# Kernel optimization log

Hardware: AMD Instinct MI355X
Metric: run time of the kernel (lower is better)

The kernel has to match this reference:

```python
import jax, jax.numpy as jnp
import numpy as np

B, N, NPOINT, NSAMPLE = 8, 4096, 1024, 32
IN_CH = 29
MLP = [64, 64, 128]
D_IN = IN_CH + 3  # 32
D_OUT = 128
EPS = 1e-5


def setup_inputs() -> dict:
    key = jax.random.key(0)
    ks = jax.random.split(key, 32)
    inp = {}
    inp["xyz"] = jax.random.normal(ks[0], (B, 3, N), jnp.float32)
    inp["points"] = jax.random.normal(ks[1], (B, IN_CH, N), jnp.float32)
    last = IN_CH + 3
    for i, oc in enumerate(MLP):
        inp[f"mlp_w{i}"] = jax.random.normal(ks[2 + i], (oc, last), jnp.float32) * np.sqrt(2.0 / last).astype(np.float32)
        inp[f"mlp_b{i}"] = jnp.zeros((oc,), jnp.float32)
        inp[f"mlp_g{i}"] = jnp.ones((oc,), jnp.float32)
        inp[f"mlp_be{i}"] = jnp.zeros((oc,), jnp.float32)
        last = oc
    inp["conv1_w"] = jax.random.normal(ks[10], (D_OUT // 2, 4), jnp.float32) * np.float32(np.sqrt(2.0 / 4))
    inp["conv1_b"] = jnp.zeros((D_OUT // 2,), jnp.float32)
    inp["bn1_g"] = jnp.ones((D_OUT // 2,), jnp.float32)
    inp["bn1_be"] = jnp.zeros((D_OUT // 2,), jnp.float32)
    inp["conv2_w"] = jax.random.normal(ks[11], (D_OUT // 2, D_IN), jnp.float32) * np.float32(np.sqrt(2.0 / D_IN))
    inp["conv2_b"] = jnp.zeros((D_OUT // 2,), jnp.float32)
    inp["bn2_g"] = jnp.ones((D_OUT // 2,), jnp.float32)
    inp["bn2_be"] = jnp.zeros((D_OUT // 2,), jnp.float32)
    return inp


def _conv1x1(x, w, b):
    # x: [B,Cin,ns,S], w: [Cout,Cin] -> [B,Cout,ns,S]
    return jnp.einsum("bcns,oc->bons", x, w) + b[None, :, None, None]


def _bn_relu(x, g, be):
    # training-mode BatchNorm2d: batch stats over (B, ns, S), biased variance
    m = jnp.mean(x, axis=(0, 2, 3), keepdims=True)
    v = jnp.var(x, axis=(0, 2, 3), keepdims=True)
    y = g[None, :, None, None] * (x - m) * jax.lax.rsqrt(v + EPS) + be[None, :, None, None]
    return jax.nn.relu(y)


def _fps(xyz):
    # xyz: [B,N,3] -> centroid indices [B,NPOINT]; deterministic start at index 0
    Bn, Nn, _ = xyz.shape

    def step(carry, _):
        dist, far = carry
        cen = jnp.take_along_axis(xyz, far[:, None, None], axis=1)  # [B,1,3]
        d = jnp.sum((xyz - cen) ** 2, axis=-1)                      # [B,N]
        dist = jnp.minimum(dist, d)
        new_far = jnp.argmax(dist, axis=-1).astype(jnp.int32)
        return (dist, new_far), far

    init = (jnp.full((Bn, Nn), 1e10, xyz.dtype), jnp.zeros((Bn,), jnp.int32))
    _, cents = jax.lax.scan(step, init, None, length=NPOINT)
    return cents.T  # [B,NPOINT]


def _forward(xyz, points, mlp_params, conv1_w, conv1_b, bn1_g, bn1_be,
             conv2_w, conv2_b, bn2_g, bn2_be):
    xyz_t = xyz.transpose(0, 2, 1)      # [B,N,3]
    pts_t = points.transpose(0, 2, 1)   # [B,N,C]
    xyz_sg = jax.lax.stop_gradient(xyz_t)

    ct_idx = _fps(xyz_sg)                                   # [B,S]
    bidx = jnp.arange(B)[:, None]
    ct_xyz = xyz_t[bidx, ct_idx]                            # [B,S,3]

    # kNN via squared distances (indices only -> stop_gradient)
    ct_sg = jax.lax.stop_gradient(ct_xyz)
    d2 = (jnp.sum(ct_sg ** 2, -1)[:, :, None]
          + jnp.sum(xyz_sg ** 2, -1)[:, None, :]
          - 2.0 * jnp.einsum("bsc,bnc->bsn", ct_sg, xyz_sg))  # [B,S,N]
    _, gidx = jax.lax.top_k(-d2, NSAMPLE)                     # [B,S,ns]

    bidx3 = jnp.arange(B)[:, None, None]
    grouped_xyz = xyz_t[bidx3, gidx]                          # [B,S,ns,3]
    ft_xyz = grouped_xyz - ct_xyz[:, :, None, :]              # [B,S,ns,3]
    ft_points = jnp.concatenate([ft_xyz, pts_t[bidx3, gidx]], axis=-1)  # [B,S,ns,3+C]
    ft = ft_points.transpose(0, 3, 2, 1)                      # [B,3+C,ns,S]

    # shared MLP (conv-bn-relu stack), then max over neighbors
    x = ft
    for (w, b, g, be) in mlp_params:
        x = _bn_relu(_conv1x1(x, w, b), g, be)
    new_points1 = jnp.max(x, axis=2)                          # [B,mlp[-1],S]

    # relative positional encoding branch
    ct_p = ct_xyz.transpose(0, 2, 1)                          # [B,3,S]
    grouped_p = grouped_xyz.transpose(0, 3, 2, 1)             # [B,3,ns,S]
    rel = grouped_p - ct_p[:, :, None, :]                     # [B,3,ns,S]
    rd = jnp.sqrt(jnp.maximum(jnp.sum(rel ** 2, axis=1, keepdims=True), 1e-12))
    new_xyz = _bn_relu(_conv1x1(jnp.concatenate([rel, rd], axis=1), conv1_w, conv1_b), bn1_g, bn1_be)
    new_pts = _bn_relu(_conv1x1(ft, conv2_w, conv2_b), bn2_g, bn2_be)

    f_concat = jnp.concatenate([new_xyz, new_pts], axis=1)    # [B,d_out,ns,S]
    new_points2 = jnp.concatenate([jnp.mean(f_concat, axis=2), jnp.max(f_concat, axis=2)], axis=1)
    conv_points = jnp.concatenate([new_points1, new_points2], axis=1)  # [B,mlp[-1]+2*d_out,S]
    return ct_p, conv_points


def reference(xyz, points,
              mlp_w0, mlp_b0, mlp_g0, mlp_be0,
              mlp_w1, mlp_b1, mlp_g1, mlp_be1,
              mlp_w2, mlp_b2, mlp_g2, mlp_be2,
              conv1_w, conv1_b, bn1_g, bn1_be,
              conv2_w, conv2_b, bn2_g, bn2_be):
    mlp_params = [(mlp_w0, mlp_b0, mlp_g0, mlp_be0),
                  (mlp_w1, mlp_b1, mlp_g1, mlp_be1),
                  (mlp_w2, mlp_b2, mlp_g2, mlp_be2)]
    return _forward(xyz, points, mlp_params, conv1_w, conv1_b, bn1_g, bn1_be,
                    conv2_w, conv2_b, bn2_g, bn2_be)
```

## Files before the change

kernel.cpp:

```cpp
#include <hip/hip_runtime.h>
#include <cfloat>
#include <math.h>

constexpr int B_ = 8, N_ = 4096, S_ = 1024, NS_ = 32;
constexpr int R_ = B_ * S_ * NS_;
constexpr float EPS_ = 1e-5f;

__global__ __launch_bounds__(512) void fps_kernel(const float* __restrict__ xyz,
                                                  int* __restrict__ ct_idx) {
    int b = blockIdx.x;
    const float* xb = xyz + (size_t)b * 3 * N_;
    int t = threadIdx.x;
    __shared__ float sx[N_], sy[N_], sz[N_];
    __shared__ unsigned long long sb[2][8];
    for (int i = t; i < N_; i += 512) {
        sx[i] = xb[i];
        sy[i] = xb[N_ + i];
        sz[i] = xb[2 * N_ + i];
    }
    float px[8], py[8], pz[8], dist[8];
    unsigned inv_idx[8];
#pragma unroll
    for (int j = 0; j < 8; j++) {
        int n = j * 512 + t;
        px[j] = xb[n];
        py[j] = xb[N_ + n];
        pz[j] = xb[2 * N_ + n];
        dist[j] = 1e10f;
        inv_idx[j] = ~(unsigned)n;
    }
    __syncthreads();
    float cx = sx[0], cy = sy[0], cz = sz[0];
    int far = 0;
    for (int it = 0; it < S_; it++) {
        if (t == 0) ct_idx[b * S_ + it] = far;
        unsigned long long best = 0ull;
#pragma unroll
        for (int j = 0; j < 8; j++) {
            float dx = px[j] - cx, dy = py[j] - cy, dz = pz[j] - cz;
            float d = dx * dx + dy * dy + dz * dz;
            dist[j] = fminf(dist[j], d);
            unsigned long long pk =
                ((unsigned long long)__float_as_uint(dist[j]) << 32) | inv_idx[j];
            best = pk > best ? pk : best;
        }
#pragma unroll
        for (int m = 1; m < 64; m <<= 1) {
            unsigned long long o = __shfl_xor(best, m);
            best = o > best ? o : best;
        }
        int p = it & 1;
        if ((t & 63) == 0) sb[p][t >> 6] = best;
        __syncthreads();
#pragma unroll
        for (int w = 0; w < 8; w++) {
            unsigned long long o = sb[p][w];
            best = o > best ? o : best;
        }
        far = (int)(~(unsigned)(best & 0xffffffffu));
        cx = sx[far]; cy = sy[far]; cz = sz[far];
    }
}

__global__ __launch_bounds__(256) void knn_kernel(const float* __restrict__ xyz,
                                                  const int* __restrict__ ct_idx,
                                                  int* __restrict__ gidx) {
    int bs = blockIdx.x;
    int b = bs >> 10;
    const float* xb = xyz + (size_t)b * 3 * N_;
    int ci = ct_idx[bs];
    float cx = xb[ci], cy = xb[N_ + ci], cz = xb[2 * N_ + ci];
    float cs = cx * cx + cy * cy + cz * cz;
    int t = threadIdx.x;
    float val[16];
#pragma unroll
    for (int j = 0; j < 16; j++) {
        int n = j * 256 + t;
        float x = xb[n], y = xb[N_ + n], z = xb[2 * N_ + n];
        float xn = x * x + y * y + z * z;
        float dot = cx * x + cy * y + cz * z;
        val[j] = cs + xn - 2.f * dot;
    }
    __shared__ float sv[4];
    __shared__ int si[4];
    int out_base = bs * NS_;
    for (int iter = 0; iter < NS_; iter++) {
        float bv = FLT_MAX; int bi = 1 << 30;
#pragma unroll
        for (int j = 0; j < 16; j++) {
            if (val[j] < bv) { bv = val[j]; bi = j * 256 + t; }
        }
#pragma unroll
        for (int m = 1; m < 64; m <<= 1) {
            float ov = __shfl_xor(bv, m); int oi = __shfl_xor(bi, m);
            if (ov < bv || (ov == bv && oi < bi)) { bv = ov; bi = oi; }
        }
        if ((t & 63) == 0) { sv[t >> 6] = bv; si[t >> 6] = bi; }
        __syncthreads();
        bv = sv[0]; bi = si[0];
#pragma unroll
        for (int w = 1; w < 4; w++) {
            float ov = sv[w]; int oi = si[w];
            if (ov < bv || (ov == bv && oi < bi)) { bv = ov; bi = oi; }
        }
        if (t == 0) gidx[out_base + iter] = bi;
        if ((bi & 255) == t) val[bi >> 8] = FLT_MAX;
        __syncthreads();
    }
}

__global__ __launch_bounds__(256) void ctp_kernel(const float* __restrict__ xyz,
                                                  const int* __restrict__ ct_idx,
                                                  float* __restrict__ out) {
    int i = blockIdx.x * 256 + threadIdx.x;
    if (i >= B_ * 3 * S_) return;
    int b = i / (3 * S_);
    int rem = i - b * 3 * S_;
    int c = rem >> 10;
    int s = rem & (S_ - 1);
    int ci = ct_idx[b * S_ + s];
    out[i] = xyz[(size_t)b * 3 * N_ + (size_t)c * N_ + ci];
}

__global__ __launch_bounds__(256) void gather_kernel(const float* __restrict__ xyz,
                                                     const float* __restrict__ pts,
                                                     const int* __restrict__ ct_idx,
                                                     const int* __restrict__ gidx,
                                                     float* __restrict__ ft) {
    int r = blockIdx.x * 256 + threadIdx.x;
    int b = r >> 15;
    int s = (r >> 5) & (S_ - 1);
    int g = gidx[r];
    int ci = ct_idx[b * S_ + s];
    const float* xb = xyz + (size_t)b * 3 * N_;
    float rx = xb[g] - xb[ci];
    float ry = xb[N_ + g] - xb[N_ + ci];
    float rz = xb[2 * N_ + g] - xb[2 * N_ + ci];
    ft[r] = rx;
    ft[(size_t)R_ + r] = ry;
    ft[(size_t)2 * R_ + r] = rz;
    float rd = sqrtf(fmaxf(rx * rx + ry * ry + rz * rz, 1e-12f));
    ft[(size_t)32 * R_ + r] = rd;
    const float* pb = pts + (size_t)b * 29 * N_;
#pragma unroll
    for (int c = 0; c < 29; c++) ft[(size_t)(3 + c) * R_ + r] = pb[(size_t)c * N_ + g];
}

template <int CIN, bool AFF>
__global__ __launch_bounds__(256) void convk(const float* __restrict__ xin,
                                             const float* __restrict__ W,
                                             const float* __restrict__ bias,
                                             const float* __restrict__ ab,
                                             float* __restrict__ out0,
                                             float* __restrict__ out1) {
    __shared__ float Ws[CIN][64];
    __shared__ float bs[64];
    __shared__ float as_[CIN], bbs[CIN];
    int oc0 = blockIdx.y * 64;
    for (int i = threadIdx.x; i < CIN * 64; i += 256) {
        int o = i & 63, c = i >> 6;
        Ws[c][o] = W[(size_t)(oc0 + o) * CIN + c];
    }
    if (threadIdx.x < 64) bs[threadIdx.x] = bias[oc0 + threadIdx.x];
    if (AFF) {
        for (int i = threadIdx.x; i < CIN; i += 256) { as_[i] = ab[i]; bbs[i] = ab[CIN + i]; }
    }
    __syncthreads();
    size_t r0 = (size_t)blockIdx.x * 512 + threadIdx.x;
    float acc0[64], acc1[64];
#pragma unroll
    for (int o = 0; o < 64; o++) { acc0[o] = 0.f; acc1[o] = 0.f; }
    for (int c = 0; c < CIN; c++) {
        float x0 = xin[(size_t)c * R_ + r0];
        float x1 = xin[(size_t)c * R_ + r0 + 256];
        if (AFF) {
            float a = as_[c], bb = bbs[c];
            x0 = fmaxf(fmaf(a, x0, bb), 0.f);
            x1 = fmaxf(fmaf(a, x1, bb), 0.f);
        }
#pragma unroll
        for (int o = 0; o < 64; o++) {
            float w = Ws[c][o];
            acc0[o] = fmaf(x0, w, acc0[o]);
            acc1[o] = fmaf(x1, w, acc1[o]);
        }
    }
    float* outp = blockIdx.y ? out1 : out0;
#pragma unroll
    for (int o = 0; o < 64; o++) {
        float bv = bs[o];
        outp[(size_t)o * R_ + r0] = acc0[o] + bv;
        outp[(size_t)o * R_ + r0 + 256] = acc1[o] + bv;
    }
}

__global__ __launch_bounds__(256) void conv1_kernel(const float* __restrict__ ft,
                                                    const float* __restrict__ W,
                                                    const float* __restrict__ bias,
                                                    float* __restrict__ out) {
    __shared__ float Ws[4][64];
    __shared__ float bs[64];
    {
        int i = threadIdx.x;
        if (i < 256) { int o = i & 63, c = i >> 6; Ws[c][o] = W[o * 4 + c]; }
    }
    if (threadIdx.x < 64) bs[threadIdx.x] = bias[threadIdx.x];
    __syncthreads();
    size_t r0 = (size_t)blockIdx.x * 512 + threadIdx.x;
    float acc0[64], acc1[64];
#pragma unroll
    for (int o = 0; o < 64; o++) { acc0[o] = 0.f; acc1[o] = 0.f; }
    const int chs[4] = {0, 1, 2, 32};
#pragma unroll
    for (int c = 0; c < 4; c++) {
        int ch = chs[c];
        float x0 = ft[(size_t)ch * R_ + r0];
        float x1 = ft[(size_t)ch * R_ + r0 + 256];
#pragma unroll
        for (int o = 0; o < 64; o++) {
            float w = Ws[c][o];
            acc0[o] = fmaf(x0, w, acc0[o]);
            acc1[o] = fmaf(x1, w, acc1[o]);
        }
    }
#pragma unroll
    for (int o = 0; o < 64; o++) {
        float bv = bs[o];
        out[(size_t)o * R_ + r0] = acc0[o] + bv;
        out[(size_t)o * R_ + r0 + 256] = acc1[o] + bv;
    }
}

__global__ __launch_bounds__(256) void stats_partial(const float* __restrict__ y,
                                                     float* __restrict__ partial,
                                                     int cofs) {
    int c = blockIdx.x, p = blockIdx.y;
    const float* src = y + (size_t)c * R_ + (size_t)p * (R_ / 32);
    float s = 0.f, q = 0.f;
    for (int i = threadIdx.x; i < R_ / 32; i += 256) {
        float v = src[i];
        s += v;
        q = fmaf(v, v, q);
    }
#pragma unroll
    for (int m = 1; m < 64; m <<= 1) { s += __shfl_xor(s, m); q += __shfl_xor(q, m); }
    __shared__ float ls[4], lq[4];
    int w = threadIdx.x >> 6;
    if ((threadIdx.x & 63) == 0) { ls[w] = s; lq[w] = q; }
    __syncthreads();
    if (threadIdx.x == 0) {
        s = ls[0] + ls[1] + ls[2] + ls[3];
        q = lq[0] + lq[1] + lq[2] + lq[3];
        int idx = ((cofs + c) * 32 + p) * 2;
        partial[idx] = s;
        partial[idx + 1] = q;
    }
}

__global__ __launch_bounds__(64) void stats_final(const float* __restrict__ partial,
                                                  const float* __restrict__ g,
                                                  const float* __restrict__ be,
                                                  float* __restrict__ ab, int C) {
    int c = blockIdx.x, t = threadIdx.x;
    float s = 0.f, q = 0.f;
    if (t < 32) {
        int idx = (c * 32 + t) * 2;
        s = partial[idx];
        q = partial[idx + 1];
    }
#pragma unroll
    for (int m = 1; m < 32; m <<= 1) { s += __shfl_xor(s, m); q += __shfl_xor(q, m); }
    if (t == 0) {
        float inv = 1.0f / (float)R_;
        float mean = s * inv;
        float var = q * inv - mean * mean;
        float a = g[c] / sqrtf(var + EPS_);
        ab[c] = a;
        ab[C + c] = be[c] - mean * a;
    }
}

__global__ __launch_bounds__(128) void final_max(const float* __restrict__ yA,
                                                 const float* __restrict__ yC,
                                                 const float* __restrict__ ab,
                                                 float* __restrict__ out) {
    int bs = blockIdx.x;
    int c = threadIdx.x;
    const float* src = (c < 64 ? yA + (size_t)c * R_ : yC + (size_t)(c - 64) * R_) + (size_t)bs * NS_;
    float a = ab[c], bb = ab[128 + c];
    const float4* s4 = reinterpret_cast<const float4*>(src);
    float m = -FLT_MAX;
#pragma unroll
    for (int i = 0; i < 8; i++) {
        float4 v = s4[i];
        m = fmaxf(m, fmaxf(fmaf(a, v.x, bb), 0.f));
        m = fmaxf(m, fmaxf(fmaf(a, v.y, bb), 0.f));
        m = fmaxf(m, fmaxf(fmaf(a, v.z, bb), 0.f));
        m = fmaxf(m, fmaxf(fmaf(a, v.w, bb), 0.f));
    }
    int b = bs >> 10, s = bs & (S_ - 1);
    out[24576 + (size_t)b * 393216 + (size_t)c * 1024 + s] = m;
}

__global__ __launch_bounds__(128) void final_meanmax(const float* __restrict__ z1,
                                                     const float* __restrict__ z2,
                                                     const float* __restrict__ ab1,
                                                     const float* __restrict__ ab2,
                                                     float* __restrict__ out) {
    int bs = blockIdx.x;
    int c = threadIdx.x;
    const float* src;
    float a, bb;
    if (c < 64) { src = z1 + (size_t)c * R_; a = ab1[c]; bb = ab1[64 + c]; }
    else        { src = z2 + (size_t)(c - 64) * R_; a = ab2[c - 64]; bb = ab2[64 + (c - 64)]; }
    src += (size_t)bs * NS_;
    const float4* s4 = reinterpret_cast<const float4*>(src);
    float m = -FLT_MAX, sm = 0.f;
#pragma unroll
    for (int i = 0; i < 8; i++) {
        float4 v = s4[i];
        float t0 = fmaxf(fmaf(a, v.x, bb), 0.f); sm += t0; m = fmaxf(m, t0);
        float t1 = fmaxf(fmaf(a, v.y, bb), 0.f); sm += t1; m = fmaxf(m, t1);
        float t2 = fmaxf(fmaf(a, v.z, bb), 0.f); sm += t2; m = fmaxf(m, t2);
        float t3 = fmaxf(fmaf(a, v.w, bb), 0.f); sm += t3; m = fmaxf(m, t3);
    }
    int b = bs >> 10, s = bs & (S_ - 1);
    size_t ob = 24576 + (size_t)b * 393216;
    out[ob + (size_t)(128 + c) * 1024 + s] = sm * 0.03125f;
    out[ob + (size_t)(256 + c) * 1024 + s] = m;
}

extern "C" void kernel_launch(void* const* d_in, const int* in_sizes, int n_in,
                              void* d_out, int out_size, void* d_ws, size_t ws_size,
                              hipStream_t stream) {
    const float* xyz = (const float*)d_in[0];
    const float* pts = (const float*)d_in[1];
    const float* W0 = (const float*)d_in[2];  const float* b0 = (const float*)d_in[3];
    const float* g0 = (const float*)d_in[4];  const float* be0 = (const float*)d_in[5];
    const float* W1 = (const float*)d_in[6];  const float* b1 = (const float*)d_in[7];
    const float* g1 = (const float*)d_in[8];  const float* be1 = (const float*)d_in[9];
    const float* W2 = (const float*)d_in[10]; const float* b2 = (const float*)d_in[11];
    const float* g2 = (const float*)d_in[12]; const float* be2 = (const float*)d_in[13];
    const float* c1w = (const float*)d_in[14]; const float* c1b = (const float*)d_in[15];
    const float* bg1 = (const float*)d_in[16]; const float* bbe1 = (const float*)d_in[17];
    const float* c2w = (const float*)d_in[18]; const float* c2b = (const float*)d_in[19];
    const float* bg2 = (const float*)d_in[20]; const float* bbe2 = (const float*)d_in[21];
    float* out = (float*)d_out;

    int* ct_idx = (int*)d_ws;
    int* gidx = ct_idx + B_ * S_;
    float* fbase = (float*)d_ws;
    float* ft = fbase + 270336;
    float* A = ft + (size_t)33 * R_;
    float* Bb = A + (size_t)64 * R_;
    float* C = Bb + (size_t)64 * R_;
    float* partial = C + (size_t)64 * R_;
    float* ab0 = partial + 8192;
    float* ab1 = ab0 + 128;
    float* ab2 = ab1 + 128;
    float* abz1 = ab2 + 256;
    float* abz2 = abz1 + 128;

    fps_kernel<<<B_, 512, 0, stream>>>(xyz, ct_idx);
    knn_kernel<<<B_ * S_, 256, 0, stream>>>(xyz, ct_idx, gidx);
    ctp_kernel<<<(B_ * 3 * S_ + 255) / 256, 256, 0, stream>>>(xyz, ct_idx, out);
    gather_kernel<<<R_ / 256, 256, 0, stream>>>(xyz, pts, ct_idx, gidx, ft);

    convk<32, false><<<dim3(R_ / 512, 1), 256, 0, stream>>>(ft, W0, b0, nullptr, A, nullptr);
    stats_partial<<<dim3(64, 32), 256, 0, stream>>>(A, partial, 0);
    stats_final<<<64, 64, 0, stream>>>(partial, g0, be0, ab0, 64);
    convk<64, true><<<dim3(R_ / 512, 1), 256, 0, stream>>>(A, W1, b1, ab0, Bb, nullptr);
    stats_partial<<<dim3(64, 32), 256, 0, stream>>>(Bb, partial, 0);
    stats_final<<<64, 64, 0, stream>>>(partial, g1, be1, ab1, 64);
    convk<64, true><<<dim3(R_ / 512, 2), 256, 0, stream>>>(Bb, W2, b2, ab1, A, C);
    stats_partial<<<dim3(64, 32), 256, 0, stream>>>(A, partial, 0);
    stats_partial<<<dim3(64, 32), 256, 0, stream>>>(C, partial, 64);
    stats_final<<<128, 64, 0, stream>>>(partial, g2, be2, ab2, 128);
    final_max<<<B_ * S_, 128, 0, stream>>>(A, C, ab2, out);

    convk<32, false><<<dim3(R_ / 512, 1), 256, 0, stream>>>(ft, c2w, c2b, nullptr, Bb, nullptr);
    stats_partial<<<dim3(64, 32), 256, 0, stream>>>(Bb, partial, 0);
    stats_final<<<64, 64, 0, stream>>>(partial, bg2, bbe2, abz2, 64);

    conv1_kernel<<<R_ / 512, 256, 0, stream>>>(ft, c1w, c1b, A);
    stats_partial<<<dim3(64, 32), 256, 0, stream>>>(A, partial, 0);
    stats_final<<<64, 64, 0, stream>>>(partial, bg1, bbe1, abz1, 64);

    final_meanmax<<<B_ * S_, 128, 0, stream>>>(A, Bb, abz1, abz2, out);
}
```

Before: 1.675 ms.

## Rework FPS argmax reduction with DPP wave max and min-index pass

The farthest-point-sampling kernel now runs 256 threads with 16 points each instead of 512 threads with 8. The 64-bit packed shuffle argmax is replaced by a two-pass 32-bit reduction: first a DPP wave max of the distance, then a DPP wave min of the indices that match that max. The per-iteration latency chain in the serial FPS loop is meant to shrink, with fewer waves taking part in the block barrier. In exchange each thread does more work, and the DPP row/broadcast control values have to produce a correct full-wave result in lane 63.

```diff
diff --git a/kernel.cpp b/kernel.cpp
--- a/kernel.cpp
+++ b/kernel.cpp
@@ -6,57 +6,86 @@
 constexpr int R_ = B_ * S_ * NS_;
 constexpr float EPS_ = 1e-5f;
 
-__global__ __launch_bounds__(512) void fps_kernel(const float* __restrict__ xyz,
+__device__ __forceinline__ unsigned dpp_red_umax(unsigned x) {
+    unsigned t;
+#define STEP_(ctrl) t = (unsigned)__builtin_amdgcn_update_dpp((int)x, (int)x, ctrl, 0xf, 0xf, false); x = x > t ? x : t;
+    STEP_(0x111) STEP_(0x112) STEP_(0x114) STEP_(0x118) STEP_(0x142) STEP_(0x143)
+#undef STEP_
+    return x;
+}
+__device__ __forceinline__ unsigned dpp_red_umin(unsigned x) {
+    unsigned t;
+#define STEP_(ctrl) t = (unsigned)__builtin_amdgcn_update_dpp((int)x, (int)x, ctrl, 0xf, 0xf, false); x = x < t ? x : t;
+    STEP_(0x111) STEP_(0x112) STEP_(0x114) STEP_(0x118) STEP_(0x142) STEP_(0x143)
+#undef STEP_
+    return x;
+}
+
+__global__ __launch_bounds__(256) void fps_kernel(const float* __restrict__ xyz,
                                                   int* __restrict__ ct_idx) {
     int b = blockIdx.x;
     const float* xb = xyz + (size_t)b * 3 * N_;
     int t = threadIdx.x;
     __shared__ float sx[N_], sy[N_], sz[N_];
-    __shared__ unsigned long long sb[2][8];
-    for (int i = t; i < N_; i += 512) {
+    __shared__ unsigned long long sb[2][4];
+    for (int i = t; i < N_; i += 256) {
         sx[i] = xb[i];
         sy[i] = xb[N_ + i];
         sz[i] = xb[2 * N_ + i];
     }
-    float px[8], py[8], pz[8], dist[8];
-    unsigned inv_idx[8];
-#pragma unroll
-    for (int j = 0; j < 8; j++) {
-        int n = j * 512 + t;
+    float px[16], py[16], pz[16], dist[16];
+#pragma unroll
+    for (int j = 0; j < 16; j++) {
+        int n = j * 256 + t;
         px[j] = xb[n];
         py[j] = xb[N_ + n];
         pz[j] = xb[2 * N_ + n];
         dist[j] = 1e10f;
-        inv_idx[j] = ~(unsigned)n;
     }
     __syncthreads();
     float cx = sx[0], cy = sy[0], cz = sz[0];
     int far = 0;
+    int w = t >> 6;
     for (int it = 0; it < S_; it++) {
         if (t == 0) ct_idx[b * S_ + it] = far;
-        unsigned long long best = 0ull;
+#pragma unroll
+        for (int j = 0; j < 16; j++) {
+            float dx = px[j] - cx, dy = py[j] - cy, dz = pz[j] - cz;
+            float d = dx * dx;
+            d = fmaf(dy, dy, d);
+            d = fmaf(dz, dz, d);
+            dist[j] = fminf(dist[j], d);
+        }
+        float m8[8], m4[4];
+#pragma unroll
+        for (int j = 0; j < 8; j++) m8[j] = fmaxf(dist[2 * j], dist[2 * j + 1]);
+#pragma unroll
+        for (int j = 0; j < 4; j++) m4[j] = fmaxf(m8[2 * j], m8[2 * j + 1]);
+        float lmax = fmaxf(fmaxf(m4[0], m4[1]), fmaxf(m4[2], m4[3]));
+        unsigned wmax = (unsigned)__builtin_amdgcn_readlane(
+            (int)dpp_red_umax(__float_as_uint(lmax)), 63);
+        unsigned c8[8], c4[4];
 #pragma unroll
         for (int j = 0; j < 8; j++) {
-            float dx = px[j] - cx, dy = py[j] - cy, dz = pz[j] - cz;
-            float d = dx * dx + dy * dy + dz * dz;
-            dist[j] = fminf(dist[j], d);
-            unsigned long long pk =
-                ((unsigned long long)__float_as_uint(dist[j]) << 32) | inv_idx[j];
-            best = pk > best ? pk : best;
-        }
-#pragma unroll
-        for (int m = 1; m < 64; m <<= 1) {
-            unsigned long long o = __shfl_xor(best, m);
-            best = o > best ? o : best;
-        }
+            unsigned a = (__float_as_uint(dist[2 * j]) == wmax)
+                             ? (unsigned)((2 * j) * 256 + t) : 0xffffffffu;
+            unsigned bq = (__float_as_uint(dist[2 * j + 1]) == wmax)
+                             ? (unsigned)((2 * j + 1) * 256 + t) : 0xffffffffu;
+            c8[j] = a < bq ? a : bq;
+        }
+#pragma unroll
+        for (int j = 0; j < 4; j++) c4[j] = c8[2 * j] < c8[2 * j + 1] ? c8[2 * j] : c8[2 * j + 1];
+        unsigned c01 = c4[0] < c4[1] ? c4[0] : c4[1];
+        unsigned c23 = c4[2] < c4[3] ? c4[2] : c4[3];
+        unsigned mn = dpp_red_umin(c01 < c23 ? c01 : c23);
         int p = it & 1;
-        if ((t & 63) == 0) sb[p][t >> 6] = best;
+        if ((t & 63) == 63)
+            sb[p][w] = ((unsigned long long)wmax << 32) | (unsigned)(~mn);
         __syncthreads();
-#pragma unroll
-        for (int w = 0; w < 8; w++) {
-            unsigned long long o = sb[p][w];
-            best = o > best ? o : best;
-        }
+        unsigned long long b0 = sb[p][0], b1 = sb[p][1], b2 = sb[p][2], b3 = sb[p][3];
+        unsigned long long m01 = b0 > b1 ? b0 : b1;
+        unsigned long long m23 = b2 > b3 ? b2 : b3;
+        unsigned long long best = m01 > m23 ? m01 : m23;
         far = (int)(~(unsigned)(best & 0xffffffffu));
         cx = sx[far]; cy = sy[far]; cz = sz[far];
     }
@@ -361,7 +390,7 @@
     float* abz1 = ab2 + 256;
     float* abz2 = abz1 + 128;
 
-    fps_kernel<<<B_, 512, 0, stream>>>(xyz, ct_idx);
+    fps_kernel<<<B_, 256, 0, stream>>>(xyz, ct_idx);
     knn_kernel<<<B_ * S_, 256, 0, stream>>>(xyz, ct_idx, gidx);
     ctp_kernel<<<(B_ * 3 * S_ + 255) / 256, 256, 0, stream>>>(xyz, ct_idx, out);
     gather_kernel<<<R_ / 256, 256, 0, stream>>>(xyz, pts, ct_idx, gidx, ft);
```

Measured after the change: 1.430 ms. 1.17x faster.

## Fuse BN statistics into conv epilogues and use DPP reductions in FPS/kNN

Applied to the files above, without the earlier changes.

Removes the separate stats_partial passes by computing per-channel sum and sum-of-squares in the conv and conv1 epilogues. Each wave reduces them with DPP row operations, and one partial per block is written for a smaller statsf kernel to finish. This avoids re-reading each large activation tensor from memory just to get BN statistics. FPS and kNN reductions are also moved to DPP-based 64-bit packed max/min with a tree pre-reduction, and kNN drops one barrier per iteration by double-buffering shared memory. The costs are extra register pressure in the conv epilogue and a different order of floating-point summation.

```diff
diff --git a/kernel.cpp b/kernel.cpp
--- a/kernel.cpp
+++ b/kernel.cpp
@@ -5,6 +5,32 @@
 constexpr int B_ = 8, N_ = 4096, S_ = 1024, NS_ = 32;
 constexpr int R_ = B_ * S_ * NS_;
 constexpr float EPS_ = 1e-5f;
+
+__device__ __forceinline__ void dpp_max_u64(unsigned& hi, unsigned& lo) {
+#define STEP_(ctrl) { \
+    unsigned h2 = (unsigned)__builtin_amdgcn_update_dpp((int)hi, (int)hi, ctrl, 0xf, 0xf, false); \
+    unsigned l2 = (unsigned)__builtin_amdgcn_update_dpp((int)lo, (int)lo, ctrl, 0xf, 0xf, false); \
+    if (h2 > hi || (h2 == hi && l2 > lo)) { hi = h2; lo = l2; } }
+    STEP_(0x111) STEP_(0x112) STEP_(0x114) STEP_(0x118) STEP_(0x142) STEP_(0x143)
+#undef STEP_
+}
+__device__ __forceinline__ void dpp_min_u64(unsigned& hi, unsigned& lo) {
+#define STEP_(ctrl) { \
+    unsigned h2 = (unsigned)__builtin_amdgcn_update_dpp((int)hi, (int)hi, ctrl, 0xf, 0xf, false); \
+    unsigned l2 = (unsigned)__builtin_amdgcn_update_dpp((int)lo, (int)lo, ctrl, 0xf, 0xf, false); \
+    if (h2 < hi || (h2 == hi && l2 < lo)) { hi = h2; lo = l2; } }
+    STEP_(0x111) STEP_(0x112) STEP_(0x114) STEP_(0x118) STEP_(0x142) STEP_(0x143)
+#undef STEP_
+}
+__device__ __forceinline__ float dpp_sum_f32(float x) {
+#define ADD_(ctrl, rm) { \
+    int t_ = __builtin_amdgcn_update_dpp(0, __float_as_int(x), ctrl, rm, 0xf, true); \
+    x += __int_as_float(t_); }
+    ADD_(0x111, 0xf) ADD_(0x112, 0xf) ADD_(0x114, 0xf) ADD_(0x118, 0xf)
+    ADD_(0x142, 0xa) ADD_(0x143, 0xc)
+#undef ADD_
+    return x;
+}
 
 __global__ __launch_bounds__(512) void fps_kernel(const float* __restrict__ xyz,
                                                   int* __restrict__ ct_idx) {
@@ -19,7 +45,7 @@
         sz[i] = xb[2 * N_ + i];
     }
     float px[8], py[8], pz[8], dist[8];
-    unsigned inv_idx[8];
+    unsigned inv[8];
 #pragma unroll
     for (int j = 0; j < 8; j++) {
         int n = j * 512 + t;
@@ -27,37 +53,46 @@
         py[j] = xb[N_ + n];
         pz[j] = xb[2 * N_ + n];
         dist[j] = 1e10f;
-        inv_idx[j] = ~(unsigned)n;
+        inv[j] = ~(unsigned)n;
     }
     __syncthreads();
     float cx = sx[0], cy = sy[0], cz = sz[0];
     int far = 0;
+    int w = t >> 6;
     for (int it = 0; it < S_; it++) {
         if (t == 0) ct_idx[b * S_ + it] = far;
-        unsigned long long best = 0ull;
+        unsigned long long pk[8];
 #pragma unroll
         for (int j = 0; j < 8; j++) {
             float dx = px[j] - cx, dy = py[j] - cy, dz = pz[j] - cz;
-            float d = dx * dx + dy * dy + dz * dz;
+            float d = dx * dx;
+            d = fmaf(dy, dy, d);
+            d = fmaf(dz, dz, d);
             dist[j] = fminf(dist[j], d);
-            unsigned long long pk =
-                ((unsigned long long)__float_as_uint(dist[j]) << 32) | inv_idx[j];
-            best = pk > best ? pk : best;
+            pk[j] = ((unsigned long long)__float_as_uint(dist[j]) << 32) | inv[j];
         }
-#pragma unroll
-        for (int m = 1; m < 64; m <<= 1) {
-            unsigned long long o = __shfl_xor(best, m);
-            best = o > best ? o : best;
-        }
+        unsigned long long m4a = pk[0] > pk[1] ? pk[0] : pk[1];
+        unsigned long long m4b = pk[2] > pk[3] ? pk[2] : pk[3];
+        unsigned long long m4c = pk[4] > pk[5] ? pk[4] : pk[5];
+        unsigned long long m4d = pk[6] > pk[7] ? pk[6] : pk[7];
+        unsigned long long m2a = m4a > m4b ? m4a : m4b;
+        unsigned long long m2b = m4c > m4d ? m4c : m4d;
+        unsigned long long best = m2a > m2b ? m2a : m2b;
+        unsigned hi = (unsigned)(best >> 32), lo = (unsigned)best;
+        dpp_max_u64(hi, lo);
         int p = it & 1;
-        if ((t & 63) == 0) sb[p][t >> 6] = best;
+        if ((t & 63) == 63) sb[p][w] = ((unsigned long long)hi << 32) | lo;
         __syncthreads();
-#pragma unroll
-        for (int w = 0; w < 8; w++) {
-            unsigned long long o = sb[p][w];
-            best = o > best ? o : best;
-        }
-        far = (int)(~(unsigned)(best & 0xffffffffu));
+        unsigned long long b0 = sb[p][0], b1 = sb[p][1], b2 = sb[p][2], b3 = sb[p][3];
+        unsigned long long b4 = sb[p][4], b5 = sb[p][5], b6 = sb[p][6], b7 = sb[p][7];
+        unsigned long long ma = b0 > b1 ? b0 : b1;
+        unsigned long long mb = b2 > b3 ? b2 : b3;
+        unsigned long long mc = b4 > b5 ? b4 : b5;
+        unsigned long long md = b6 > b7 ? b6 : b7;
+        unsigned long long me = ma > mb ? ma : mb;
+        unsigned long long mf = mc > md ? mc : md;
+        unsigned long long bw = me > mf ? me : mf;
+        far = (int)(~(unsigned)(bw & 0xffffffffu));
         cx = sx[far]; cy = sy[far]; cz = sz[far];
     }
 }
@@ -72,40 +107,42 @@
     float cx = xb[ci], cy = xb[N_ + ci], cz = xb[2 * N_ + ci];
     float cs = cx * cx + cy * cy + cz * cz;
     int t = threadIdx.x;
-    float val[16];
+    unsigned long long pk[16];
 #pragma unroll
     for (int j = 0; j < 16; j++) {
         int n = j * 256 + t;
         float x = xb[n], y = xb[N_ + n], z = xb[2 * N_ + n];
         float xn = x * x + y * y + z * z;
         float dot = cx * x + cy * y + cz * z;
-        val[j] = cs + xn - 2.f * dot;
-    }
-    __shared__ float sv[4];
-    __shared__ int si[4];
+        float val = cs + xn - 2.f * dot;
+        unsigned vb = __float_as_uint(val);
+        unsigned key = (vb & 0x80000000u) ? ~vb : (vb | 0x80000000u);
+        pk[j] = ((unsigned long long)key << 32) | (unsigned)n;
+    }
+    __shared__ unsigned long long sw[2][4];
     int out_base = bs * NS_;
+    int w = t >> 6;
     for (int iter = 0; iter < NS_; iter++) {
-        float bv = FLT_MAX; int bi = 1 << 30;
-#pragma unroll
-        for (int j = 0; j < 16; j++) {
-            if (val[j] < bv) { bv = val[j]; bi = j * 256 + t; }
-        }
-#pragma unroll
-        for (int m = 1; m < 64; m <<= 1) {
-            float ov = __shfl_xor(bv, m); int oi = __shfl_xor(bi, m);
-            if (ov < bv || (ov == bv && oi < bi)) { bv = ov; bi = oi; }
-        }
-        if ((t & 63) == 0) { sv[t >> 6] = bv; si[t >> 6] = bi; }
+        unsigned long long m8[8], m4[4];
+#pragma unroll
+        for (int j = 0; j < 8; j++) m8[j] = pk[2 * j] < pk[2 * j + 1] ? pk[2 * j] : pk[2 * j + 1];
+#pragma unroll
+        for (int j = 0; j < 4; j++) m4[j] = m8[2 * j] < m8[2 * j + 1] ? m8[2 * j] : m8[2 * j + 1];
+        unsigned long long ma = m4[0] < m4[1] ? m4[0] : m4[1];
+        unsigned long long mb = m4[2] < m4[3] ? m4[2] : m4[3];
+        unsigned long long best = ma < mb ? ma : mb;
+        unsigned hi = (unsigned)(best >> 32), lo = (unsigned)best;
+        dpp_min_u64(hi, lo);
+        int p = iter & 1;
+        if ((t & 63) == 63) sw[p][w] = ((unsigned long long)hi << 32) | lo;
         __syncthreads();
-        bv = sv[0]; bi = si[0];
-#pragma unroll
-        for (int w = 1; w < 4; w++) {
-            float ov = sv[w]; int oi = si[w];
-            if (ov < bv || (ov == bv && oi < bi)) { bv = ov; bi = oi; }
-        }
-        if (t == 0) gidx[out_base + iter] = bi;
-        if ((bi & 255) == t) val[bi >> 8] = FLT_MAX;
-        __syncthreads();
+        unsigned long long b0 = sw[p][0], b1 = sw[p][1], b2 = sw[p][2], b3 = sw[p][3];
+        unsigned long long wa = b0 < b1 ? b0 : b1;
+        unsigned long long wb = b2 < b3 ? b2 : b3;
+        unsigned long long bw = wa < wb ? wa : wb;
+        int n = (int)(unsigned)(bw & 0xffffffffu);
+        if (t == 0) gidx[out_base + iter] = n;
+        if ((n & 255) == t) pk[n >> 8] = 0xFFFFFFFF00000000ull | (unsigned)n;
     }
 }
 
@@ -152,16 +189,18 @@
                                              const float* __restrict__ bias,
                                              const float* __restrict__ ab,
                                              float* __restrict__ out0,
-                                             float* __restrict__ out1) {
+                                             float* __restrict__ out1,
+                                             float* __restrict__ partial) {
     __shared__ float Ws[CIN][64];
-    __shared__ float bs[64];
+    __shared__ float bs_[64];
     __shared__ float as_[CIN], bbs[CIN];
+    __shared__ float red[4][64][2];
     int oc0 = blockIdx.y * 64;
     for (int i = threadIdx.x; i < CIN * 64; i += 256) {
         int o = i & 63, c = i >> 6;
         Ws[c][o] = W[(size_t)(oc0 + o) * CIN + c];
     }
-    if (threadIdx.x < 64) bs[threadIdx.x] = bias[oc0 + threadIdx.x];
+    if (threadIdx.x < 64) bs_[threadIdx.x] = bias[oc0 + threadIdx.x];
     if (AFF) {
         for (int i = threadIdx.x; i < CIN; i += 256) { as_[i] = ab[i]; bbs[i] = ab[CIN + i]; }
     }
@@ -186,25 +225,43 @@
         }
     }
     float* outp = blockIdx.y ? out1 : out0;
+    int wv = threadIdx.x >> 6;
 #pragma unroll
     for (int o = 0; o < 64; o++) {
-        float bv = bs[o];
-        outp[(size_t)o * R_ + r0] = acc0[o] + bv;
-        outp[(size_t)o * R_ + r0 + 256] = acc1[o] + bv;
+        float bv = bs_[o];
+        float y0 = acc0[o] + bv;
+        float y1 = acc1[o] + bv;
+        outp[(size_t)o * R_ + r0] = y0;
+        outp[(size_t)o * R_ + r0 + 256] = y1;
+        float s = y0 + y1;
+        float q = fmaf(y0, y0, y1 * y1);
+        s = dpp_sum_f32(s);
+        q = dpp_sum_f32(q);
+        if ((threadIdx.x & 63) == 63) { red[wv][o][0] = s; red[wv][o][1] = q; }
+    }
+    __syncthreads();
+    if (threadIdx.x < 64) {
+        int o = threadIdx.x;
+        float s = red[0][o][0] + red[1][o][0] + red[2][o][0] + red[3][o][0];
+        float q = red[0][o][1] + red[1][o][1] + red[2][o][1] + red[3][o][1];
+        partial[(size_t)(oc0 + o) * 1024 + blockIdx.x] = s;
+        partial[(size_t)(oc0 + o) * 1024 + 512 + blockIdx.x] = q;
     }
 }
 
 __global__ __launch_bounds__(256) void conv1_kernel(const float* __restrict__ ft,
                                                     const float* __restrict__ W,
                                                     const float* __restrict__ bias,
-                                                    float* __restrict__ out) {
+                                                    float* __restrict__ out,
+                                                    float* __restrict__ partial) {
     __shared__ float Ws[4][64];
-    __shared__ float bs[64];
+    __shared__ float bs_[64];
+    __shared__ float red[4][64][2];
     {
         int i = threadIdx.x;
         if (i < 256) { int o = i & 63, c = i >> 6; Ws[c][o] = W[o * 4 + c]; }
     }
-    if (threadIdx.x < 64) bs[threadIdx.x] = bias[threadIdx.x];
+    if (threadIdx.x < 64) bs_[threadIdx.x] = bias[threadIdx.x];
     __syncthreads();
     size_t r0 = (size_t)blockIdx.x * 512 + threadIdx.x;
     float acc0[64], acc1[64];
@@ -223,54 +280,43 @@
             acc1[o] = fmaf(x1, w, acc1[o]);
         }
     }
+    int wv = threadIdx.x >> 6;
 #pragma unroll
     for (int o = 0; o < 64; o++) {
-        float bv = bs[o];
-        out[(size_t)o * R_ + r0] = acc0[o] + bv;
-        out[(size_t)o * R_ + r0 + 256] = acc1[o] + bv;
-    }
-}
-
-__global__ __launch_bounds__(256) void stats_partial(const float* __restrict__ y,
-                                                     float* __restrict__ partial,
-                                                     int cofs) {
-    int c = blockIdx.x, p = blockIdx.y;
-    const float* src = y + (size_t)c * R_ + (size_t)p * (R_ / 32);
-    float s = 0.f, q = 0.f;
-    for (int i = threadIdx.x; i < R_ / 32; i += 256) {
-        float v = src[i];
-        s += v;
-        q = fmaf(v, v, q);
-    }
-#pragma unroll
-    for (int m = 1; m < 64; m <<= 1) { s += __shfl_xor(s, m); q += __shfl_xor(q, m); }
-    __shared__ float ls[4], lq[4];
-    int w = threadIdx.x >> 6;
-    if ((threadIdx.x & 63) == 0) { ls[w] = s; lq[w] = q; }
+        float bv = bs_[o];
+        float y0 = acc0[o] + bv;
+        float y1 = acc1[o] + bv;
+        out[(size_t)o * R_ + r0] = y0;
+        out[(size_t)o * R_ + r0 + 256] = y1;
+        float s = y0 + y1;
+        float q = fmaf(y0, y0, y1 * y1);
+        s = dpp_sum_f32(s);
+        q = dpp_sum_f32(q);
+        if ((threadIdx.x & 63) == 63) { red[wv][o][0] = s; red[wv][o][1] = q; }
+    }
     __syncthreads();
-    if (threadIdx.x == 0) {
-        s = ls[0] + ls[1] + ls[2] + ls[3];
-        q = lq[0] + lq[1] + lq[2] + lq[3];
-        int idx = ((cofs + c) * 32 + p) * 2;
-        partial[idx] = s;
-        partial[idx + 1] = q;
-    }
-}
-
-__global__ __launch_bounds__(64) void stats_final(const float* __restrict__ partial,
-                                                  const float* __restrict__ g,
-                                                  const float* __restrict__ be,
-                                                  float* __restrict__ ab, int C) {
+    if (threadIdx.x < 64) {
+        int o = threadIdx.x;
+        float s = red[0][o][0] + red[1][o][0] + red[2][o][0] + red[3][o][0];
+        float q = red[0][o][1] + red[1][o][1] + red[2][o][1] + red[3][o][1];
+        partial[(size_t)o * 1024 + blockIdx.x] = s;
+        partial[(size_t)o * 1024 + 512 + blockIdx.x] = q;
+    }
+}
+
+__global__ __launch_bounds__(64) void statsf(const float* __restrict__ partial,
+                                             const float* __restrict__ g,
+                                             const float* __restrict__ be,
+                                             float* __restrict__ ab, int C) {
     int c = blockIdx.x, t = threadIdx.x;
     float s = 0.f, q = 0.f;
-    if (t < 32) {
-        int idx = (c * 32 + t) * 2;
-        s = partial[idx];
-        q = partial[idx + 1];
-    }
-#pragma unroll
-    for (int m = 1; m < 32; m <<= 1) { s += __shfl_xor(s, m); q += __shfl_xor(q, m); }
-    if (t == 0) {
+    for (int i = t; i < 512; i += 64) {
+        s += partial[(size_t)c * 1024 + i];
+        q += partial[(size_t)c * 1024 + 512 + i];
+    }
+    s = dpp_sum_f32(s);
+    q = dpp_sum_f32(q);
+    if (t == 63) {
         float inv = 1.0f / (float)R_;
         float mean = s * inv;
         float var = q * inv - mean * mean;
@@ -355,7 +401,7 @@
     float* Bb = A + (size_t)64 * R_;
     float* C = Bb + (size_t)64 * R_;
     float* partial = C + (size_t)64 * R_;
-    float* ab0 = partial + 8192;
+    float* ab0 = partial + 131072;
     float* ab1 = ab0 + 128;
     float* ab2 = ab1 + 128;
     float* abz1 = ab2 + 256;
@@ -366,25 +412,19 @@
     ctp_kernel<<<(B_ * 3 * S_ + 255) / 256, 256, 0, stream>>>(xyz, ct_idx, out);
     gather_kernel<<<R_ / 256, 256, 0, stream>>>(xyz, pts, ct_idx, gidx, ft);
 
-    convk<32, false><<<dim3(R_ / 512, 1), 256, 0, stream>>>(ft, W0, b0, nullptr, A, nullptr);
-    stats_partial<<<dim3(64, 32), 256, 0, stream>>>(A, partial, 0);
-    stats_final<<<64, 64, 0, stream>>>(partial, g0, be0, ab0, 64);
-    convk<64, true><<<dim3(R_ / 512, 1), 256, 0, stream>>>(A, W1, b1, ab0, Bb, nullptr);
-    stats_partial<<<dim3(64, 32), 256, 0, stream>>>(Bb, partial, 0);
-    stats_final<<<64, 64, 0, stream>>>(partial, g1, be1, ab1, 64);
-    convk<64, true><<<dim3(R_ / 512, 2), 256, 0, stream>>>(Bb, W2, b2, ab1, A, C);
-    stats_partial<<<dim3(64, 32), 256, 0, stream>>>(A, partial, 0);
-    stats_partial<<<dim3(64, 32), 256, 0, stream>>>(C, partial, 64);
-    stats_final<<<128, 64, 0, stream>>>(partial, g2, be2, ab2, 128);
+    convk<32, false><<<dim3(R_ / 512, 1), 256, 0, stream>>>(ft, W0, b0, nullptr, A, nullptr, partial);
+    statsf<<<64, 64, 0, stream>>>(partial, g0, be0, ab0, 64);
+    convk<64, true><<<dim3(R_ / 512, 1), 256, 0, stream>>>(A, W1, b1, ab0, Bb, nullptr, partial);
+    statsf<<<64, 64, 0, stream>>>(partial, g1, be1, ab1, 64);
+    convk<64, true><<<dim3(R_ / 512, 2), 256, 0, stream>>>(Bb, W2, b2, ab1, A, C, partial);
+    statsf<<<128, 64, 0, stream>>>(partial, g2, be2, ab2, 128);
     final_max<<<B_ * S_, 128, 0, stream>>>(A, C, ab2, out);
 
-    convk<32, false><<<dim3(R_ / 512, 1), 256, 0, stream>>>(ft, c2w, c2b, nullptr, Bb, nullptr);
-    stats_partial<<<dim3(64, 32), 256, 0, stream>>>(Bb, partial, 0);
-    stats_final<<<64, 64, 0, stream>>>(partial, bg2, bbe2, abz2, 64);
-
-    conv1_kernel<<<R_ / 512, 256, 0, stream>>>(ft, c1w, c1b, A);
-    stats_partial<<<dim3(64, 32), 256, 0, stream>>>(A, partial, 0);
-    stats_final<<<64, 64, 0, stream>>>(partial, bg1, bbe1, abz1, 64);
+    convk<32, false><<<dim3(R_ / 512, 1), 256, 0, stream>>>(ft, c2w, c2b, nullptr, Bb, nullptr, partial);
+    statsf<<<64, 64, 0, stream>>>(partial, bg2, bbe2, abz2, 64);
+
+    conv1_kernel<<<R_ / 512, 256, 0, stream>>>(ft, c1w, c1b, A, partial);
+    statsf<<<64, 64, 0, stream>>>(partial, bg1, bbe1, abz1, 64);
 
     final_meanmax<<<B_ * S_, 128, 0, stream>>>(A, Bb, abz1, abz2, out);
 }
```

Result: faster. 1.559 ms (-6.9%).
